# Kernel tuning notes

Hardware: AMD Instinct MI355X
Metric: run time of the kernel (lower is better)

## Reference

```python
import jax, jax.numpy as jnp
import numpy as np

B, T, D = 2, 2048, 1024
N, H = 16, 64  # num_heads, head_dim


def setup_inputs() -> dict:
    key = jax.random.key(0)
    ks = jax.random.split(key, 8)
    glorot = lambda k, shape, fan_in, fan_out: jax.random.uniform(
        k, shape, jnp.float32, -1.0, 1.0) * np.sqrt(6.0 / (fan_in + fan_out))
    return {
        "q": jax.random.normal(ks[0], (B, T, D), jnp.float32),
        "v": jax.random.normal(ks[1], (B, T, D), jnp.float32),
        "k": jax.random.normal(ks[2], (B, T, D), jnp.float32),
        "w_query": glorot(ks[3], (D, N, H), D, N * H),
        "b_query": jnp.zeros((N, 1, H), jnp.float32),
        "w_value": glorot(ks[4], (D, N, H), D, N * H),
        "b_value": jnp.zeros((N, 1, H), jnp.float32),
        "w_key": glorot(ks[5], (D, N, H), D, N * H),
        "b_key": jnp.zeros((N, 1, H), jnp.float32),
        "w_projection": glorot(ks[6], (N, D, H), N * H, D),
        "b_projection": jnp.zeros((1, D), jnp.float32),
    }


def reference(q, v, k, w_query, b_query, w_value, b_value, w_key, b_key,
              w_projection, b_projection):
    # QKV projections: [B,T,D] x [D,N,H] -> [B,N,T,H]
    query = jnp.einsum('btd,dnh->bnth', q, w_query) + b_query
    value = jnp.einsum('btd,dnh->bnth', v, w_value) + b_value
    key_p = jnp.einsum('btd,dnh->bnth', k, w_key) + b_key
    # Scaled dot-product attention, scores divided by sqrt(head_dim)
    scale = 1.0 / jnp.sqrt(jnp.asarray(H, query.dtype))
    scores = jnp.einsum('bnth,bnsh->bnts', query, key_p) * scale  # [B,N,T,T]
    weights = jax.nn.softmax(scores, axis=-1)
    attn = jnp.einsum('bnts,bnsh->bnth', weights, value)
    # Output projection: [B,N,T,H] x [N,D,H] -> [B,T,D]
    out = jnp.einsum('bnth,ndh->btd', attn, w_projection) + b_projection
    return out
```

## Files before the change

### kernel.cpp

```cpp
#include <hip/hip_runtime.h>
#include <hip/hip_bf16.h>
#include <cstdint>
#include <cstddef>


typedef __attribute__((ext_vector_type(8))) short short8;
typedef __attribute__((ext_vector_type(4))) float floatx4;
typedef __attribute__((ext_vector_type(8))) unsigned short ushort8;

#define EXP2F(x) __builtin_amdgcn_exp2f(x)

static __device__ __forceinline__ unsigned short f2bf(float f) {
    union { float f; unsigned int u; } v; v.f = f;
    unsigned int r = v.u + 0x7fffu + ((v.u >> 16) & 1u);
    return (unsigned short)(r >> 16);
}
static __device__ __forceinline__ unsigned int pk2bf(float lo, float hi) {
    __hip_bfloat162 t = __float22bfloat162_rn(make_float2(lo, hi));
    union { __hip_bfloat162 h; unsigned int u; } c; c.h = t;
    return c.u;
}
static __device__ __forceinline__ void gl_lds16(const unsigned short* g, unsigned short* l) {
    __builtin_amdgcn_global_load_lds(
        (const __attribute__((address_space(1))) unsigned int*)g,
        (__attribute__((address_space(3))) unsigned int*)l, 16, 0, 0);
}

__global__ __launch_bounds__(256) void mha_transpose_w(
    const float* __restrict__ wq, const float* __restrict__ wk, const float* __restrict__ wv,
    unsigned short* __restrict__ wqT, unsigned short* __restrict__ wkT, unsigned short* __restrict__ wvT)
{
    __shared__ float tile[32][33];
    const float* src; unsigned short* dst;
    int z = blockIdx.z;
    if (z == 0)      { src = wq; dst = wqT; }
    else if (z == 1) { src = wk; dst = wkT; }
    else             { src = wv; dst = wvT; }
    int n0 = blockIdx.x * 32, d0 = blockIdx.y * 32;
    int tx = threadIdx.x, ty = threadIdx.y;
    #pragma unroll
    for (int j = 0; j < 4; ++j)
        tile[ty + j * 8][tx] = src[(size_t)(d0 + ty + j * 8) * 1024 + n0 + tx];
    __syncthreads();
    #pragma unroll
    for (int j = 0; j < 4; ++j)
        dst[(size_t)(n0 + ty + j * 8) * 1024 + d0 + tx] = f2bf(tile[tx][ty + j * 8]);
}

__global__ __launch_bounds__(256) void mha_reorder_wp(
    const float* __restrict__ wp, unsigned short* __restrict__ wp2)
{
    int base = blockIdx.x * 1024 + threadIdx.x;
    #pragma unroll
    for (int i = 0; i < 4; ++i) {
        int idx = base + i * 256;
        int n = idx >> 16, d = (idx >> 6) & 1023, h = idx & 63;
        wp2[(size_t)d * 1024 + n * 64 + h] = f2bf(wp[idx]);
    }
}

__global__ __launch_bounds__(256) void prep_bf16_3(
    const float* __restrict__ x0, const float* __restrict__ x1, const float* __restrict__ x2,
    unsigned short* __restrict__ o0, unsigned short* __restrict__ o1, unsigned short* __restrict__ o2)
{
    int y = blockIdx.y;
    const float* x = y == 0 ? x0 : (y == 1 ? x1 : x2);
    unsigned short* o = y == 0 ? o0 : (y == 1 ? o1 : o2);
    size_t i = ((size_t)blockIdx.x * 256 + threadIdx.x) * 8;
    float4 a = *(const float4*)(x + i);
    float4 b = *(const float4*)(x + i + 4);
    uint4 pk;
    pk.x = pk2bf(a.x, a.y); pk.y = pk2bf(a.z, a.w);
    pk.z = pk2bf(b.x, b.y); pk.w = pk2bf(b.z, b.w);
    *(uint4*)(o + i) = pk;
}

__global__ __launch_bounds__(256) void gemm_qkv128(
    const unsigned short* __restrict__ A0, const unsigned short* __restrict__ A1,
    const unsigned short* __restrict__ A2,
    const unsigned short* __restrict__ W0, const unsigned short* __restrict__ W1,
    const unsigned short* __restrict__ W2,
    const float* __restrict__ b0, const float* __restrict__ b1, const float* __restrict__ b2,
    unsigned short* __restrict__ O0, unsigned short* __restrict__ O1, unsigned short* __restrict__ O2,
    float qscale, int matSel)
{
    __shared__ unsigned short As[128 * 32];
    __shared__ unsigned short Bs[128 * 32];
    int bm = blockIdx.x, by = blockIdx.y;
    int mat, nt;
    if (matSel < 0) { mat = by >> 3; nt = by & 7; } else { mat = matSel; nt = by; }
    const unsigned short* A  = mat == 0 ? A0 : (mat == 1 ? A1 : A2);
    const unsigned short* WT = mat == 0 ? W0 : (mat == 1 ? W1 : W2);
    const float* bias        = mat == 0 ? b0 : (mat == 1 ? b1 : b2);
    unsigned short* Out      = mat == 0 ? O0 : (mat == 1 ? O1 : O2);
    float scale = (mat == 0) ? qscale : 1.0f;
    int vmode = (mat == 2);

    int tid = threadIdx.x;
    int w = tid >> 6, lane = tid & 63, c15 = lane & 15, quad = lane >> 4;
    int wm = w >> 1, wn = w & 1;

    const unsigned short* gA[2]; unsigned short* lA[2];
    const unsigned short* gB[2]; unsigned short* lB[2];
    #pragma unroll
    for (int i = 0; i < 2; ++i) {
        int s = (w * 2 + i) * 64 + lane;
        gA[i] = A  + (size_t)(bm * 128 + (s >> 2)) * 1024 + (s & 3) * 8;
        lA[i] = &As[s * 8];
        gB[i] = WT + (size_t)(nt * 128 + (s >> 2)) * 1024 + (s & 3) * 8;
        lB[i] = &Bs[s * 8];
    }

    floatx4 acc[4][4];
    #pragma unroll
    for (int mi = 0; mi < 4; ++mi)
        #pragma unroll
        for (int ni = 0; ni < 4; ++ni) acc[mi][ni] = (floatx4){0.f, 0.f, 0.f, 0.f};

    for (int kt = 0; kt < 32; ++kt) {
        __syncthreads();
        #pragma unroll
        for (int i = 0; i < 2; ++i) { gl_lds16(gA[i] + kt * 32, lA[i]); gl_lds16(gB[i] + kt * 32, lB[i]); }
        __syncthreads();
        short8 af[4], bfr[4];
        #pragma unroll
        for (int mi = 0; mi < 4; ++mi)
            af[mi] = *(const short8*)&As[(wm * 64 + mi * 16 + c15) * 32 + quad * 8];
        #pragma unroll
        for (int ni = 0; ni < 4; ++ni)
            bfr[ni] = *(const short8*)&Bs[(wn * 64 + ni * 16 + c15) * 32 + quad * 8];
        #pragma unroll
        for (int mi = 0; mi < 4; ++mi)
            #pragma unroll
            for (int ni = 0; ni < 4; ++ni)
                acc[mi][ni] = __builtin_amdgcn_mfma_f32_16x16x32_bf16(af[mi], bfr[ni], acc[mi][ni], 0, 0, 0);
    }
    #pragma unroll
    for (int mi = 0; mi < 4; ++mi)
        #pragma unroll
        for (int ni = 0; ni < 4; ++ni)
            #pragma unroll
            for (int r = 0; r < 4; ++r) {
                int row = bm * 128 + wm * 64 + mi * 16 + quad * 4 + r;
                int col = nt * 128 + wn * 64 + ni * 16 + c15;
                float val = (acc[mi][ni][r] + bias[col]) * scale;
                int b = row >> 11, t = row & 2047, n = col >> 6, h = col & 63;
                if (vmode)
                    Out[((size_t)(b * 16 + n) * 64 + h) * 2048 + t] = f2bf(val);
                else
                    Out[((size_t)(b * 16 + n) * 2048 + t) * 64 + h] = f2bf(val);
            }
}

__global__ __launch_bounds__(256) void mha_flash3(
    const unsigned short* __restrict__ Qp, const unsigned short* __restrict__ Kp,
    const unsigned short* __restrict__ Vt, unsigned short* __restrict__ attnb)
{
    __shared__ unsigned short Ks[64 * 72];
    __shared__ unsigned short Vs[64 * 72];
    __shared__ unsigned short Pl[4][32 * 72];

    int bi = blockIdx.x;
    int xcd = bi & 7, j = bi >> 3;
    int bn = xcd * 4 + (j >> 4), qt = j & 15;
    int b = bn >> 4, n = bn & 15;
    int tid = threadIdx.x;
    int w = tid >> 6, lane = tid & 63, c15 = lane & 15, quad = lane >> 4;

    const unsigned short* Qb = Qp + (size_t)bn * 2048 * 64;
    const unsigned short* Kb = Kp + (size_t)bn * 2048 * 64;
    const unsigned short* Vb = Vt + (size_t)bn * 64 * 2048;

    int qbase = qt * 128 + w * 32;

    short8 bQ[2][2];
    #pragma unroll
    for (int tni = 0; tni < 2; ++tni)
        #pragma unroll
        for (int kc = 0; kc < 2; ++kc)
            bQ[tni][kc] = *(const short8*)(Qb + (size_t)(qbase + tni * 16 + c15) * 64 + kc * 32 + quad * 8);

    float l_i[2] = {0.f, 0.f};
    floatx4 o[2][4];
    #pragma unroll
    for (int i = 0; i < 2; ++i)
        #pragma unroll
        for (int j2 = 0; j2 < 4; ++j2) o[i][j2] = (floatx4){0.f, 0.f, 0.f, 0.f};

    unsigned short* Pw = &Pl[w][0];
    int srow = tid >> 3, scc = tid & 7;

    ushort8 kreg[2], vreg[2];
    #pragma unroll
    for (int i = 0; i < 2; ++i) {
        kreg[i] = *(const ushort8*)(Kb + (size_t)(srow + i * 32) * 64 + scc * 8);
        vreg[i] = *(const ushort8*)(Vb + (size_t)(srow + i * 32) * 2048 + scc * 8);
    }

    for (int it = 0; it < 32; ++it) {
        __syncthreads();
        #pragma unroll
        for (int i = 0; i < 2; ++i) {
            *(ushort8*)&Ks[(srow + i * 32) * 72 + scc * 8] = kreg[i];
            *(ushort8*)&Vs[(srow + i * 32) * 72 + scc * 8] = vreg[i];
        }
        if (it < 31) {
            int s1 = (it + 1) * 64;
            #pragma unroll
            for (int i = 0; i < 2; ++i) {
                kreg[i] = *(const ushort8*)(Kb + (size_t)(s1 + srow + i * 32) * 64 + scc * 8);
                vreg[i] = *(const ushort8*)(Vb + (size_t)(srow + i * 32) * 2048 + s1 + scc * 8);
            }
        }
        __syncthreads();

        floatx4 sc[4][2];
        #pragma unroll
        for (int smi = 0; smi < 4; ++smi) {
            short8 a0 = *(const short8*)&Ks[(smi * 16 + c15) * 72 + quad * 8];
            short8 a1 = *(const short8*)&Ks[(smi * 16 + c15) * 72 + 32 + quad * 8];
            #pragma unroll
            for (int tni = 0; tni < 2; ++tni) {
                floatx4 t = (floatx4){0.f, 0.f, 0.f, 0.f};
                t = __builtin_amdgcn_mfma_f32_16x16x32_bf16(a0, bQ[tni][0], t, 0, 0, 0);
                t = __builtin_amdgcn_mfma_f32_16x16x32_bf16(a1, bQ[tni][1], t, 0, 0, 0);
                sc[smi][tni] = t;
            }
        }
        #pragma unroll
        for (int tni = 0; tni < 2; ++tni) {
            float rs = 0.f;
            #pragma unroll
            for (int smi = 0; smi < 4; ++smi) {
                float p0 = EXP2F(sc[smi][tni][0]);
                float p1 = EXP2F(sc[smi][tni][1]);
                float p2 = EXP2F(sc[smi][tni][2]);
                float p3 = EXP2F(sc[smi][tni][3]);
                rs += (p0 + p1) + (p2 + p3);
                uint2 pw;
                pw.x = pk2bf(p0, p1);
                pw.y = pk2bf(p2, p3);
                *(uint2*)&Pw[(tni * 16 + c15) * 72 + smi * 16 + quad * 4] = pw;
            }
            l_i[tni] += rs;
        }
        short8 bv[4][2];
        #pragma unroll
        for (int hni = 0; hni < 4; ++hni)
            #pragma unroll
            for (int kc = 0; kc < 2; ++kc)
                bv[hni][kc] = *(const short8*)&Vs[(hni * 16 + c15) * 72 + kc * 32 + quad * 8];
        #pragma unroll
        for (int tmi = 0; tmi < 2; ++tmi) {
            short8 ap0 = *(const short8*)&Pw[(tmi * 16 + c15) * 72 + quad * 8];
            short8 ap1 = *(const short8*)&Pw[(tmi * 16 + c15) * 72 + 32 + quad * 8];
            #pragma unroll
            for (int hni = 0; hni < 4; ++hni) {
                o[tmi][hni] = __builtin_amdgcn_mfma_f32_16x16x32_bf16(ap0, bv[hni][0], o[tmi][hni], 0, 0, 0);
                o[tmi][hni] = __builtin_amdgcn_mfma_f32_16x16x32_bf16(ap1, bv[hni][1], o[tmi][hni], 0, 0, 0);
            }
        }
    }
    float lf[2];
    #pragma unroll
    for (int tmi = 0; tmi < 2; ++tmi) {
        float s = l_i[tmi];
        s += __shfl_xor(s, 16, 64);
        s += __shfl_xor(s, 32, 64);
        lf[tmi] = s;
    }
    #pragma unroll
    for (int tmi = 0; tmi < 2; ++tmi)
        #pragma unroll
        for (int r = 0; r < 4; ++r) {
            float linv = 1.0f / __shfl(lf[tmi], quad * 4 + r, 64);
            int t = qbase + tmi * 16 + quad * 4 + r;
            #pragma unroll
            for (int hni = 0; hni < 4; ++hni) {
                int col = n * 64 + hni * 16 + c15;
                attnb[(size_t)(b * 2048 + t) * 1024 + col] = f2bf(o[tmi][hni][r] * linv);
            }
        }
}

__global__ __launch_bounds__(256) void gemm_out64v2(
    const unsigned short* __restrict__ A, const unsigned short* __restrict__ BT,
    const float* __restrict__ bias, float* __restrict__ out)
{
    __shared__ unsigned short As[64 * 64];
    __shared__ unsigned short Bs[128 * 64];
    int bm = blockIdx.x, nt = blockIdx.y;
    int tid = threadIdx.x;
    int w = tid >> 6, lane = tid & 63, c15 = lane & 15, quad = lane >> 4;
    int wm = w >> 1, wn = w & 1;

    const unsigned short* gA[2]; unsigned short* lA[2];
    const unsigned short* gB[4]; unsigned short* lB[4];
    #pragma unroll
    for (int i = 0; i < 2; ++i) {
        int s = (w * 2 + i) * 64 + lane;
        int row = s >> 3, cl = (s & 7) ^ (row & 7);
        gA[i] = A + (size_t)(bm * 64 + row) * 1024 + cl * 8;
        lA[i] = &As[s * 8];
    }
    #pragma unroll
    for (int i = 0; i < 4; ++i) {
        int s = (w * 4 + i) * 64 + lane;
        int row = s >> 3, cl = (s & 7) ^ (row & 7);
        gB[i] = BT + (size_t)(nt * 128 + row) * 1024 + cl * 8;
        lB[i] = &Bs[s * 8];
    }

    floatx4 acc[2][4];
    #pragma unroll
    for (int mi = 0; mi < 2; ++mi)
        #pragma unroll
        for (int ni = 0; ni < 4; ++ni) acc[mi][ni] = (floatx4){0.f, 0.f, 0.f, 0.f};

    for (int kt = 0; kt < 16; ++kt) {
        __syncthreads();
        #pragma unroll
        for (int i = 0; i < 2; ++i) gl_lds16(gA[i] + kt * 64, lA[i]);
        #pragma unroll
        for (int i = 0; i < 4; ++i) gl_lds16(gB[i] + kt * 64, lB[i]);
        __syncthreads();
        #pragma unroll
        for (int kc = 0; kc < 2; ++kc) {
            short8 af[2], bfr[4];
            #pragma unroll
            for (int mi = 0; mi < 2; ++mi) {
                int row = wm * 32 + mi * 16 + c15;
                af[mi] = *(const short8*)&As[row * 64 + (((kc * 4 + quad) ^ (row & 7)) * 8)];
            }
            #pragma unroll
            for (int ni = 0; ni < 4; ++ni) {
                int row = wn * 64 + ni * 16 + c15;
                bfr[ni] = *(const short8*)&Bs[row * 64 + (((kc * 4 + quad) ^ (row & 7)) * 8)];
            }
            #pragma unroll
            for (int mi = 0; mi < 2; ++mi)
                #pragma unroll
                for (int ni = 0; ni < 4; ++ni)
                    acc[mi][ni] = __builtin_amdgcn_mfma_f32_16x16x32_bf16(af[mi], bfr[ni], acc[mi][ni], 0, 0, 0);
        }
    }
    #pragma unroll
    for (int mi = 0; mi < 2; ++mi)
        #pragma unroll
        for (int ni = 0; ni < 4; ++ni)
            #pragma unroll
            for (int r = 0; r < 4; ++r) {
                int row = bm * 64 + wm * 32 + mi * 16 + quad * 4 + r;
                int col = nt * 128 + wn * 64 + ni * 16 + c15;
                out[(size_t)row * 1024 + col] = acc[mi][ni][r] + bias[col];
            }
}

extern "C" void kernel_launch(void* const* d_in, const int* in_sizes, int n_in,
                              void* d_out, int out_size, void* d_ws, size_t ws_size,
                              hipStream_t stream)
{
    const float* q  = (const float*)d_in[0];
    const float* v  = (const float*)d_in[1];
    const float* k  = (const float*)d_in[2];
    const float* wq = (const float*)d_in[3];
    const float* bq = (const float*)d_in[4];
    const float* wv = (const float*)d_in[5];
    const float* bv = (const float*)d_in[6];
    const float* wk = (const float*)d_in[7];
    const float* bk = (const float*)d_in[8];
    const float* wp = (const float*)d_in[9];
    const float* bp = (const float*)d_in[10];
    float* out = (float*)d_out;

    char* ws = (char*)d_ws;
    unsigned short* wqT  = (unsigned short*)(ws + (size_t)0);
    unsigned short* wkT  = (unsigned short*)(ws + ((size_t)2  << 20));
    unsigned short* wvT  = (unsigned short*)(ws + ((size_t)4  << 20));
    unsigned short* wp2  = (unsigned short*)(ws + ((size_t)6  << 20));
    unsigned short* Qp   = (unsigned short*)(ws + ((size_t)8  << 20));
    unsigned short* Kp   = (unsigned short*)(ws + ((size_t)16 << 20));
    unsigned short* Vtp  = (unsigned short*)(ws + ((size_t)24 << 20));
    unsigned short* Xb   = (unsigned short*)(ws + ((size_t)32 << 20));
    unsigned short* attnb= (unsigned short*)(ws + ((size_t)32 << 20));

    const float qscale = 0.125f * 1.44269504088896f;

    hipLaunchKernelGGL(mha_transpose_w, dim3(32, 32, 3), dim3(32, 8), 0, stream,
                       wq, wk, wv, wqT, wkT, wvT);
    hipLaunchKernelGGL(mha_reorder_wp, dim3(1024), dim3(256), 0, stream, wp, wp2);

    if (ws_size >= ((size_t)64 << 20)) {
        unsigned short* qb = (unsigned short*)(ws + ((size_t)40 << 20));
        unsigned short* kb = (unsigned short*)(ws + ((size_t)48 << 20));
        unsigned short* vb = (unsigned short*)(ws + ((size_t)56 << 20));
        hipLaunchKernelGGL(prep_bf16_3, dim3(2048, 3), dim3(256), 0, stream, q, k, v, qb, kb, vb);
        hipLaunchKernelGGL(gemm_qkv128, dim3(32, 24), dim3(256), 0, stream,
                           qb, kb, vb, wqT, wkT, wvT, bq, bk, bv, Qp, Kp, Vtp, qscale, -1);
    } else {
        hipLaunchKernelGGL(prep_bf16_3, dim3(2048, 1), dim3(256), 0, stream, q, q, q, Xb, Xb, Xb);
        hipLaunchKernelGGL(gemm_qkv128, dim3(32, 8), dim3(256), 0, stream,
                           Xb, Xb, Xb, wqT, wkT, wvT, bq, bk, bv, Qp, Kp, Vtp, qscale, 0);
        hipLaunchKernelGGL(prep_bf16_3, dim3(2048, 1), dim3(256), 0, stream, k, k, k, Xb, Xb, Xb);
        hipLaunchKernelGGL(gemm_qkv128, dim3(32, 8), dim3(256), 0, stream,
                           Xb, Xb, Xb, wqT, wkT, wvT, bq, bk, bv, Qp, Kp, Vtp, qscale, 1);
        hipLaunchKernelGGL(prep_bf16_3, dim3(2048, 1), dim3(256), 0, stream, v, v, v, Xb, Xb, Xb);
        hipLaunchKernelGGL(gemm_qkv128, dim3(32, 8), dim3(256), 0, stream,
                           Xb, Xb, Xb, wqT, wkT, wvT, bq, bk, bv, Qp, Kp, Vtp, qscale, 2);
    }

    hipLaunchKernelGGL(mha_flash3, dim3(512), dim3(256), 0, stream, Qp, Kp, Vtp, attnb);
    hipLaunchKernelGGL(gemm_out64v2, dim3(64, 8), dim3(256), 0, stream, attnb, wp2, bp, out);
}
```

Before: 226.5 us.

## Double-buffer K/V LDS tiles in flash attention loop with MFMA priority hints

Splits the K and V shared-memory tiles into two ping-pong buffers. Each step writes the next tile to the other buffer and prefetches the tile after that into registers while the current tile is consumed, so one barrier per step replaces two. It also raises wave priority around the MFMA sections with s_setprio. The cost is doubled LDS for K/V, which may reduce occupancy, plus longer register lifetimes for the prefetched data.

```diff
diff --git a/kernel.cpp b/kernel.cpp
--- a/kernel.cpp
+++ b/kernel.cpp
@@ -152,12 +152,92 @@
             }
 }
 
+static __device__ __forceinline__ void flash_step(
+    const unsigned short* KC, const unsigned short* VC,
+    unsigned short* KN, unsigned short* VN,
+    unsigned short* Pw,
+    const unsigned short* Kb, const unsigned short* Vb,
+    const short8 (&bQ)[2][2], float (&l_i)[2], floatx4 (&o)[2][4],
+    ushort8 (&kreg)[2], ushort8 (&vreg)[2],
+    int it, int c15, int quad, int srow, int scc)
+{
+    floatx4 sc[4][2];
+    __builtin_amdgcn_s_setprio(1);
+    #pragma unroll
+    for (int smi = 0; smi < 4; ++smi) {
+        short8 a0 = *(const short8*)&KC[(smi * 16 + c15) * 72 + quad * 8];
+        short8 a1 = *(const short8*)&KC[(smi * 16 + c15) * 72 + 32 + quad * 8];
+        #pragma unroll
+        for (int tni = 0; tni < 2; ++tni) {
+            floatx4 t = (floatx4){0.f, 0.f, 0.f, 0.f};
+            t = __builtin_amdgcn_mfma_f32_16x16x32_bf16(a0, bQ[tni][0], t, 0, 0, 0);
+            t = __builtin_amdgcn_mfma_f32_16x16x32_bf16(a1, bQ[tni][1], t, 0, 0, 0);
+            sc[smi][tni] = t;
+        }
+    }
+    __builtin_amdgcn_s_setprio(0);
+
+    if (it < 31) {
+        #pragma unroll
+        for (int i = 0; i < 2; ++i) {
+            *(ushort8*)&KN[(srow + i * 32) * 72 + scc * 8] = kreg[i];
+            *(ushort8*)&VN[(srow + i * 32) * 72 + scc * 8] = vreg[i];
+        }
+        if (it < 30) {
+            int s2 = (it + 2) * 64;
+            #pragma unroll
+            for (int i = 0; i < 2; ++i) {
+                kreg[i] = *(const ushort8*)(Kb + (size_t)(s2 + srow + i * 32) * 64 + scc * 8);
+                vreg[i] = *(const ushort8*)(Vb + (size_t)(srow + i * 32) * 2048 + s2 + scc * 8);
+            }
+        }
+    }
+
+    #pragma unroll
+    for (int tni = 0; tni < 2; ++tni) {
+        float rs = 0.f;
+        #pragma unroll
+        for (int smi = 0; smi < 4; ++smi) {
+            float p0 = EXP2F(sc[smi][tni][0]);
+            float p1 = EXP2F(sc[smi][tni][1]);
+            float p2 = EXP2F(sc[smi][tni][2]);
+            float p3 = EXP2F(sc[smi][tni][3]);
+            rs += (p0 + p1) + (p2 + p3);
+            uint2 pw;
+            pw.x = pk2bf(p0, p1);
+            pw.y = pk2bf(p2, p3);
+            *(uint2*)&Pw[(tni * 16 + c15) * 72 + smi * 16 + quad * 4] = pw;
+        }
+        l_i[tni] += rs;
+    }
+
+    short8 bv[4][2];
+    #pragma unroll
+    for (int hni = 0; hni < 4; ++hni)
+        #pragma unroll
+        for (int kc = 0; kc < 2; ++kc)
+            bv[hni][kc] = *(const short8*)&VC[(hni * 16 + c15) * 72 + kc * 32 + quad * 8];
+    __builtin_amdgcn_s_setprio(1);
+    #pragma unroll
+    for (int tmi = 0; tmi < 2; ++tmi) {
+        short8 ap0 = *(const short8*)&Pw[(tmi * 16 + c15) * 72 + quad * 8];
+        short8 ap1 = *(const short8*)&Pw[(tmi * 16 + c15) * 72 + 32 + quad * 8];
+        #pragma unroll
+        for (int hni = 0; hni < 4; ++hni) {
+            o[tmi][hni] = __builtin_amdgcn_mfma_f32_16x16x32_bf16(ap0, bv[hni][0], o[tmi][hni], 0, 0, 0);
+            o[tmi][hni] = __builtin_amdgcn_mfma_f32_16x16x32_bf16(ap1, bv[hni][1], o[tmi][hni], 0, 0, 0);
+        }
+    }
+    __builtin_amdgcn_s_setprio(0);
+    __syncthreads();
+}
+
 __global__ __launch_bounds__(256) void mha_flash3(
     const unsigned short* __restrict__ Qp, const unsigned short* __restrict__ Kp,
     const unsigned short* __restrict__ Vt, unsigned short* __restrict__ attnb)
 {
-    __shared__ unsigned short Ks[64 * 72];
-    __shared__ unsigned short Vs[64 * 72];
+    __shared__ unsigned short Ks0[64 * 72], Ks1[64 * 72];
+    __shared__ unsigned short Vs0[64 * 72], Vs1[64 * 72];
     __shared__ unsigned short Pl[4][32 * 72];
 
     int bi = blockIdx.x;
@@ -196,71 +276,26 @@
         kreg[i] = *(const ushort8*)(Kb + (size_t)(srow + i * 32) * 64 + scc * 8);
         vreg[i] = *(const ushort8*)(Vb + (size_t)(srow + i * 32) * 2048 + scc * 8);
     }
-
-    for (int it = 0; it < 32; ++it) {
-        __syncthreads();
-        #pragma unroll
-        for (int i = 0; i < 2; ++i) {
-            *(ushort8*)&Ks[(srow + i * 32) * 72 + scc * 8] = kreg[i];
-            *(ushort8*)&Vs[(srow + i * 32) * 72 + scc * 8] = vreg[i];
-        }
-        if (it < 31) {
-            int s1 = (it + 1) * 64;
-            #pragma unroll
-            for (int i = 0; i < 2; ++i) {
-                kreg[i] = *(const ushort8*)(Kb + (size_t)(s1 + srow + i * 32) * 64 + scc * 8);
-                vreg[i] = *(const ushort8*)(Vb + (size_t)(srow + i * 32) * 2048 + s1 + scc * 8);
-            }
-        }
-        __syncthreads();
-
-        floatx4 sc[4][2];
-        #pragma unroll
-        for (int smi = 0; smi < 4; ++smi) {
-            short8 a0 = *(const short8*)&Ks[(smi * 16 + c15) * 72 + quad * 8];
-            short8 a1 = *(const short8*)&Ks[(smi * 16 + c15) * 72 + 32 + quad * 8];
-            #pragma unroll
-            for (int tni = 0; tni < 2; ++tni) {
-                floatx4 t = (floatx4){0.f, 0.f, 0.f, 0.f};
-                t = __builtin_amdgcn_mfma_f32_16x16x32_bf16(a0, bQ[tni][0], t, 0, 0, 0);
-                t = __builtin_amdgcn_mfma_f32_16x16x32_bf16(a1, bQ[tni][1], t, 0, 0, 0);
-                sc[smi][tni] = t;
-            }
-        }
-        #pragma unroll
-        for (int tni = 0; tni < 2; ++tni) {
-            float rs = 0.f;
-            #pragma unroll
-            for (int smi = 0; smi < 4; ++smi) {
-                float p0 = EXP2F(sc[smi][tni][0]);
-                float p1 = EXP2F(sc[smi][tni][1]);
-                float p2 = EXP2F(sc[smi][tni][2]);
-                float p3 = EXP2F(sc[smi][tni][3]);
-                rs += (p0 + p1) + (p2 + p3);
-                uint2 pw;
-                pw.x = pk2bf(p0, p1);
-                pw.y = pk2bf(p2, p3);
-                *(uint2*)&Pw[(tni * 16 + c15) * 72 + smi * 16 + quad * 4] = pw;
-            }
-            l_i[tni] += rs;
-        }
-        short8 bv[4][2];
-        #pragma unroll
-        for (int hni = 0; hni < 4; ++hni)
-            #pragma unroll
-            for (int kc = 0; kc < 2; ++kc)
-                bv[hni][kc] = *(const short8*)&Vs[(hni * 16 + c15) * 72 + kc * 32 + quad * 8];
-        #pragma unroll
-        for (int tmi = 0; tmi < 2; ++tmi) {
-            short8 ap0 = *(const short8*)&Pw[(tmi * 16 + c15) * 72 + quad * 8];
-            short8 ap1 = *(const short8*)&Pw[(tmi * 16 + c15) * 72 + 32 + quad * 8];
-            #pragma unroll
-            for (int hni = 0; hni < 4; ++hni) {
-                o[tmi][hni] = __builtin_amdgcn_mfma_f32_16x16x32_bf16(ap0, bv[hni][0], o[tmi][hni], 0, 0, 0);
-                o[tmi][hni] = __builtin_amdgcn_mfma_f32_16x16x32_bf16(ap1, bv[hni][1], o[tmi][hni], 0, 0, 0);
-            }
-        }
-    }
+    #pragma unroll
+    for (int i = 0; i < 2; ++i) {
+        *(ushort8*)&Ks0[(srow + i * 32) * 72 + scc * 8] = kreg[i];
+        *(ushort8*)&Vs0[(srow + i * 32) * 72 + scc * 8] = vreg[i];
+    }
+    #pragma unroll
+    for (int i = 0; i < 2; ++i) {
+        kreg[i] = *(const ushort8*)(Kb + (size_t)(64 + srow + i * 32) * 64 + scc * 8);
+        vreg[i] = *(const ushort8*)(Vb + (size_t)(srow + i * 32) * 2048 + 64 + scc * 8);
+    }
+    __syncthreads();
+
+    #pragma unroll 1
+    for (int it2 = 0; it2 < 16; ++it2) {
+        flash_step(Ks0, Vs0, Ks1, Vs1, Pw, Kb, Vb, bQ, l_i, o, kreg, vreg,
+                   2 * it2,     c15, quad, srow, scc);
+        flash_step(Ks1, Vs1, Ks0, Vs0, Pw, Kb, Vb, bQ, l_i, o, kreg, vreg,
+                   2 * it2 + 1, c15, quad, srow, scc);
+    }
+
     float lf[2];
     #pragma unroll
     for (int tmi = 0; tmi < 2; ++tmi) {
```

After: 227.2 us. Within noise of the previous version (+0.3%).

## Halve flash-attention query tile, double grid, and transpose V via separate kernel

Applied to the files above, without the earlier changes.

The attention kernel now processes 64 queries per block (16 per wave) instead of 128, doubling the grid to 1024 blocks and adding occupancy hints and MFMA priority bumps. The QKV GEMM no longer scatters V in transposed layout (strided 2-byte stores); instead it writes V row-major and a new tiled LDS transpose kernel produces Vt. This aims to improve CU occupancy and store coalescing, at the cost of re-reading K/V twice as often per query and an extra kernel launch plus V round trip.

```diff
diff --git a/kernel.cpp b/kernel.cpp
--- a/kernel.cpp
+++ b/kernel.cpp
@@ -75,6 +75,26 @@
     *(uint4*)(o + i) = pk;
 }
 
+__global__ __launch_bounds__(256) void mha_tr_v(
+    const unsigned short* __restrict__ Vp, unsigned short* __restrict__ Vt)
+{
+    __shared__ unsigned short tile[64][72];
+    int bn = blockIdx.x, tb = blockIdx.y;
+    int tid = threadIdx.x;
+    const unsigned short* src = Vp + ((size_t)bn * 2048 + tb * 64) * 64;
+    unsigned short* dst = Vt + (size_t)bn * 64 * 2048 + tb * 64;
+    int r = tid >> 2, cq = (tid & 3) * 16;
+    *(ushort8*)&tile[r][cq]     = *(const ushort8*)(src + r * 64 + cq);
+    *(ushort8*)&tile[r][cq + 8] = *(const ushort8*)(src + r * 64 + cq + 8);
+    __syncthreads();
+    int h = tid >> 2, t0 = (tid & 3) * 16;
+    ushort8 o0, o1;
+    #pragma unroll
+    for (int j = 0; j < 8; ++j) { o0[j] = tile[t0 + j][h]; o1[j] = tile[t0 + 8 + j][h]; }
+    *(ushort8*)(dst + (size_t)h * 2048 + t0)     = o0;
+    *(ushort8*)(dst + (size_t)h * 2048 + t0 + 8) = o1;
+}
+
 __global__ __launch_bounds__(256) void gemm_qkv128(
     const unsigned short* __restrict__ A0, const unsigned short* __restrict__ A1,
     const unsigned short* __restrict__ A2,
@@ -82,7 +102,7 @@
     const unsigned short* __restrict__ W2,
     const float* __restrict__ b0, const float* __restrict__ b1, const float* __restrict__ b2,
     unsigned short* __restrict__ O0, unsigned short* __restrict__ O1, unsigned short* __restrict__ O2,
-    float qscale, int matSel)
+    float qscale, int matSel, int scatterV)
 {
     __shared__ unsigned short As[128 * 32];
     __shared__ unsigned short Bs[128 * 32];
@@ -94,7 +114,7 @@
     const float* bias        = mat == 0 ? b0 : (mat == 1 ? b1 : b2);
     unsigned short* Out      = mat == 0 ? O0 : (mat == 1 ? O1 : O2);
     float scale = (mat == 0) ? qscale : 1.0f;
-    int vmode = (mat == 2);
+    int vmode = (mat == 2) && scatterV;
 
     int tid = threadIdx.x;
     int w = tid >> 6, lane = tid & 63, c15 = lane & 15, quad = lane >> 4;
@@ -152,17 +172,17 @@
             }
 }
 
-__global__ __launch_bounds__(256) void mha_flash3(
+__global__ __launch_bounds__(256, 4) void mha_flash3(
     const unsigned short* __restrict__ Qp, const unsigned short* __restrict__ Kp,
     const unsigned short* __restrict__ Vt, unsigned short* __restrict__ attnb)
 {
     __shared__ unsigned short Ks[64 * 72];
     __shared__ unsigned short Vs[64 * 72];
-    __shared__ unsigned short Pl[4][32 * 72];
+    __shared__ unsigned short Pl[4][16 * 72];
 
     int bi = blockIdx.x;
     int xcd = bi & 7, j = bi >> 3;
-    int bn = xcd * 4 + (j >> 4), qt = j & 15;
+    int bn = xcd * 4 + (j >> 5), qt = j & 31;
     int b = bn >> 4, n = bn & 15;
     int tid = threadIdx.x;
     int w = tid >> 6, lane = tid & 63, c15 = lane & 15, quad = lane >> 4;
@@ -171,21 +191,17 @@
     const unsigned short* Kb = Kp + (size_t)bn * 2048 * 64;
     const unsigned short* Vb = Vt + (size_t)bn * 64 * 2048;
 
-    int qbase = qt * 128 + w * 32;
-
-    short8 bQ[2][2];
-    #pragma unroll
-    for (int tni = 0; tni < 2; ++tni)
-        #pragma unroll
-        for (int kc = 0; kc < 2; ++kc)
-            bQ[tni][kc] = *(const short8*)(Qb + (size_t)(qbase + tni * 16 + c15) * 64 + kc * 32 + quad * 8);
-
-    float l_i[2] = {0.f, 0.f};
-    floatx4 o[2][4];
-    #pragma unroll
-    for (int i = 0; i < 2; ++i)
-        #pragma unroll
-        for (int j2 = 0; j2 < 4; ++j2) o[i][j2] = (floatx4){0.f, 0.f, 0.f, 0.f};
+    int qbase = qt * 64 + w * 16;
+
+    short8 bQ[2];
+    #pragma unroll
+    for (int kc = 0; kc < 2; ++kc)
+        bQ[kc] = *(const short8*)(Qb + (size_t)(qbase + c15) * 64 + kc * 32 + quad * 8);
+
+    float l_i = 0.f;
+    floatx4 o[4];
+    #pragma unroll
+    for (int j2 = 0; j2 < 4; ++j2) o[j2] = (floatx4){0.f, 0.f, 0.f, 0.f};
 
     unsigned short* Pw = &Pl[w][0];
     int srow = tid >> 3, scc = tid & 7;
@@ -214,73 +230,68 @@
         }
         __syncthreads();
 
-        floatx4 sc[4][2];
+        floatx4 sc[4];
+        __builtin_amdgcn_s_setprio(1);
         #pragma unroll
         for (int smi = 0; smi < 4; ++smi) {
             short8 a0 = *(const short8*)&Ks[(smi * 16 + c15) * 72 + quad * 8];
             short8 a1 = *(const short8*)&Ks[(smi * 16 + c15) * 72 + 32 + quad * 8];
-            #pragma unroll
-            for (int tni = 0; tni < 2; ++tni) {
-                floatx4 t = (floatx4){0.f, 0.f, 0.f, 0.f};
-                t = __builtin_amdgcn_mfma_f32_16x16x32_bf16(a0, bQ[tni][0], t, 0, 0, 0);
-                t = __builtin_amdgcn_mfma_f32_16x16x32_bf16(a1, bQ[tni][1], t, 0, 0, 0);
-                sc[smi][tni] = t;
-            }
-        }
-        #pragma unroll
-        for (int tni = 0; tni < 2; ++tni) {
+            floatx4 t = (floatx4){0.f, 0.f, 0.f, 0.f};
+            t = __builtin_amdgcn_mfma_f32_16x16x32_bf16(a0, bQ[0], t, 0, 0, 0);
+            t = __builtin_amdgcn_mfma_f32_16x16x32_bf16(a1, bQ[1], t, 0, 0, 0);
+            sc[smi] = t;
+        }
+        __builtin_amdgcn_s_setprio(0);
+
+        {
             float rs = 0.f;
             #pragma unroll
             for (int smi = 0; smi < 4; ++smi) {
-                float p0 = EXP2F(sc[smi][tni][0]);
-                float p1 = EXP2F(sc[smi][tni][1]);
-                float p2 = EXP2F(sc[smi][tni][2]);
-                float p3 = EXP2F(sc[smi][tni][3]);
+                float p0 = EXP2F(sc[smi][0]);
+                float p1 = EXP2F(sc[smi][1]);
+                float p2 = EXP2F(sc[smi][2]);
+                float p3 = EXP2F(sc[smi][3]);
                 rs += (p0 + p1) + (p2 + p3);
                 uint2 pw;
                 pw.x = pk2bf(p0, p1);
                 pw.y = pk2bf(p2, p3);
-                *(uint2*)&Pw[(tni * 16 + c15) * 72 + smi * 16 + quad * 4] = pw;
-            }
-            l_i[tni] += rs;
-        }
+                *(uint2*)&Pw[c15 * 72 + smi * 16 + quad * 4] = pw;
+            }
+            l_i += rs;
+        }
+
         short8 bv[4][2];
         #pragma unroll
         for (int hni = 0; hni < 4; ++hni)
             #pragma unroll
             for (int kc = 0; kc < 2; ++kc)
                 bv[hni][kc] = *(const short8*)&Vs[(hni * 16 + c15) * 72 + kc * 32 + quad * 8];
-        #pragma unroll
-        for (int tmi = 0; tmi < 2; ++tmi) {
-            short8 ap0 = *(const short8*)&Pw[(tmi * 16 + c15) * 72 + quad * 8];
-            short8 ap1 = *(const short8*)&Pw[(tmi * 16 + c15) * 72 + 32 + quad * 8];
+        __builtin_amdgcn_s_setprio(1);
+        {
+            short8 ap0 = *(const short8*)&Pw[c15 * 72 + quad * 8];
+            short8 ap1 = *(const short8*)&Pw[c15 * 72 + 32 + quad * 8];
             #pragma unroll
             for (int hni = 0; hni < 4; ++hni) {
-                o[tmi][hni] = __builtin_amdgcn_mfma_f32_16x16x32_bf16(ap0, bv[hni][0], o[tmi][hni], 0, 0, 0);
-                o[tmi][hni] = __builtin_amdgcn_mfma_f32_16x16x32_bf16(ap1, bv[hni][1], o[tmi][hni], 0, 0, 0);
-            }
-        }
-    }
-    float lf[2];
-    #pragma unroll
-    for (int tmi = 0; tmi < 2; ++tmi) {
-        float s = l_i[tmi];
-        s += __shfl_xor(s, 16, 64);
-        s += __shfl_xor(s, 32, 64);
-        lf[tmi] = s;
-    }
-    #pragma unroll
-    for (int tmi = 0; tmi < 2; ++tmi)
-        #pragma unroll
-        for (int r = 0; r < 4; ++r) {
-            float linv = 1.0f / __shfl(lf[tmi], quad * 4 + r, 64);
-            int t = qbase + tmi * 16 + quad * 4 + r;
-            #pragma unroll
-            for (int hni = 0; hni < 4; ++hni) {
-                int col = n * 64 + hni * 16 + c15;
-                attnb[(size_t)(b * 2048 + t) * 1024 + col] = f2bf(o[tmi][hni][r] * linv);
-            }
-        }
+                o[hni] = __builtin_amdgcn_mfma_f32_16x16x32_bf16(ap0, bv[hni][0], o[hni], 0, 0, 0);
+                o[hni] = __builtin_amdgcn_mfma_f32_16x16x32_bf16(ap1, bv[hni][1], o[hni], 0, 0, 0);
+            }
+        }
+        __builtin_amdgcn_s_setprio(0);
+    }
+    float s = l_i;
+    s += __shfl_xor(s, 16, 64);
+    s += __shfl_xor(s, 32, 64);
+    float lf = s;
+    #pragma unroll
+    for (int r = 0; r < 4; ++r) {
+        float linv = 1.0f / __shfl(lf, quad * 4 + r, 64);
+        int t = qbase + quad * 4 + r;
+        #pragma unroll
+        for (int hni = 0; hni < 4; ++hni) {
+            int col = n * 64 + hni * 16 + c15;
+            attnb[(size_t)(b * 2048 + t) * 1024 + col] = f2bf(o[hni][r] * linv);
+        }
+    }
 }
 
 __global__ __launch_bounds__(256) void gemm_out64v2(
@@ -394,21 +405,23 @@
         unsigned short* qb = (unsigned short*)(ws + ((size_t)40 << 20));
         unsigned short* kb = (unsigned short*)(ws + ((size_t)48 << 20));
         unsigned short* vb = (unsigned short*)(ws + ((size_t)56 << 20));
+        unsigned short* Vp = Xb;
         hipLaunchKernelGGL(prep_bf16_3, dim3(2048, 3), dim3(256), 0, stream, q, k, v, qb, kb, vb);
         hipLaunchKernelGGL(gemm_qkv128, dim3(32, 24), dim3(256), 0, stream,
-                           qb, kb, vb, wqT, wkT, wvT, bq, bk, bv, Qp, Kp, Vtp, qscale, -1);
+                           qb, kb, vb, wqT, wkT, wvT, bq, bk, bv, Qp, Kp, Vp, qscale, -1, 0);
+        hipLaunchKernelGGL(mha_tr_v, dim3(32, 32), dim3(256), 0, stream, Vp, Vtp);
     } else {
         hipLaunchKernelGGL(prep_bf16_3, dim3(2048, 1), dim3(256), 0, stream, q, q, q, Xb, Xb, Xb);
         hipLaunchKernelGGL(gemm_qkv128, dim3(32, 8), dim3(256), 0, stream,
-                           Xb, Xb, Xb, wqT, wkT, wvT, bq, bk, bv, Qp, Kp, Vtp, qscale, 0);
+                           Xb, Xb, Xb, wqT, wkT, wvT, bq, bk, bv, Qp, Kp, Vtp, qscale, 0, 1);
         hipLaunchKernelGGL(prep_bf16_3, dim3(2048, 1), dim3(256), 0, stream, k, k, k, Xb, Xb, Xb);
         hipLaunchKernelGGL(gemm_qkv128, dim3(32, 8), dim3(256), 0, stream,
-                           Xb, Xb, Xb, wqT, wkT, wvT, bq, bk, bv, Qp, Kp, Vtp, qscale, 1);
+                           Xb, Xb, Xb, wqT, wkT, wvT, bq, bk, bv, Qp, Kp, Vtp, qscale, 1, 1);
         hipLaunchKernelGGL(prep_bf16_3, dim3(2048, 1), dim3(256), 0, stream, v, v, v, Xb, Xb, Xb);
         hipLaunchKernelGGL(gemm_qkv128, dim3(32, 8), dim3(256), 0, stream,
-                           Xb, Xb, Xb, wqT, wkT, wvT, bq, bk, bv, Qp, Kp, Vtp, qscale, 2);
-    }
-
-    hipLaunchKernelGGL(mha_flash3, dim3(512), dim3(256), 0, stream, Qp, Kp, Vtp, attnb);
+                           Xb, Xb, Xb, wqT, wkT, wvT, bq, bk, bv, Qp, Kp, Vtp, qscale, 2, 1);
+    }
+
+    hipLaunchKernelGGL(mha_flash3, dim3(1024), dim3(256), 0, stream, Qp, Kp, Vtp, attnb);
     hipLaunchKernelGGL(gemm_out64v2, dim3(64, 8), dim3(256), 0, stream, attnb, wp2, bp, out);
 }
```

New measurement: 237.9 us. 1.05x slower.
